# Kernel optimization log

Measured on AMD Instinct MI355X. Metric: run time of the kernel, lower is better.

The kernel has to match this reference:

```python
import jax, jax.numpy as jnp
import numpy as np

B, H, N, D = 4, 16, 2048, 64

def setup_inputs() -> dict:
    key = jax.random.key(0)
    kq, kk, kv = jax.random.split(key, 3)
    q = jax.random.normal(kq, (B, H, N, D), dtype=jnp.float32)
    k = jax.random.normal(kk, (B, H, N, D), dtype=jnp.float32)
    v = jax.random.normal(kv, (B, H, N, D), dtype=jnp.float32)
    return {"q": q, "k": k, "v": v}

def reference(q, k, v):
    scale = q.shape[-1] ** -0.5
    # sim: [b, h, i, j]
    sim = jnp.einsum('bhid,bhjd->bhij', q, k) * scale
    attn = jax.nn.softmax(sim, axis=-1)  # dropout p=0.0 -> identity
    out = jnp.einsum('bhij,bhjd->bhid', attn, v)
    return out
```

## Files before the change

kernel.cpp:

```cpp
#include <hip/hip_runtime.h>
#include <stdint.h>


#define NSEQ 2048
#define DH   64
#define BHN  64
#define NIT  32

typedef short bf16x8 __attribute__((ext_vector_type(8)));
typedef float f32x4  __attribute__((ext_vector_type(4)));
typedef float f32x16 __attribute__((ext_vector_type(16)));

__device__ __forceinline__ uint16_t f2bf(float x) {
    uint32_t u = __builtin_bit_cast(uint32_t, x);
    return (uint16_t)((u + 0x7fffu + ((u >> 16) & 1u)) >> 16);
}
__device__ __forceinline__ uint32_t pk2(float a, float b) {
    return (uint32_t)f2bf(a) | ((uint32_t)f2bf(b) << 16);
}

__global__ __launch_bounds__(256) void prepass(const float* __restrict__ K,
                                               const float* __restrict__ V,
                                               uint16_t* __restrict__ F) {
    __shared__ float T1[64 * 68];
    const int b = blockIdx.x, bh = b >> 5, kt = b & 31, t = threadIdx.x;
    const size_t gbase = ((size_t)bh * NSEQ + (size_t)kt * 64) * DH;
    const int n = t >> 2, d0 = (t & 3) * 16;
    #pragma unroll
    for (int i = 0; i < 4; ++i)
        *(float4*)&T1[n * 68 + d0 + i * 4] = *(const float4*)(V + gbase + n * 64 + d0 + i * 4);
    __syncthreads();
    uint16_t* out = F + (size_t)(bh * 32 + kt) * 8192;
    #pragma unroll
    for (int p = 0; p < 4; ++p) {
        const int e = p * 256 + t, c = e >> 6, l = e & 63;
        const int ll = l & 31, hh = l >> 5;
        float f[8];
        if (c < 8) {
            const int row = (c >> 2) * 32 + ll;
            const int col = hh * 8 + (c & 3) * 16;
            const float* kp = K + gbase + (size_t)row * 64 + col;
            float4 a = *(const float4*)(kp);
            float4 g = *(const float4*)(kp + 4);
            f[0] = a.x; f[1] = a.y; f[2] = a.z; f[3] = a.w;
            f[4] = g.x; f[5] = g.y; f[6] = g.z; f[7] = g.w;
        } else {
            const int cc = c - 8, ktg = cc >> 1;
            const int d = (cc & 1) * 32 + ll;
            #pragma unroll
            for (int j = 0; j < 8; ++j) {
                const int i = hh * 8 + j;
                const int s = (i & 3) + 8 * ((i >> 2) & 1) + 4 * ((i >> 3) & 1);
                f[j] = T1[(ktg * 16 + s) * 68 + d];
            }
        }
        uint4 o = make_uint4(pk2(f[0], f[1]), pk2(f[2], f[3]),
                             pk2(f[4], f[5]), pk2(f[6], f[7]));
        *(uint4*)(out + (size_t)c * 512 + l * 8) = o;
    }
}

__device__ __forceinline__ void load_q(const float* qp, float qscale, bf16x8 (&dst)[4]) {
    #pragma unroll
    for (int k2 = 0; k2 < 4; ++k2) {
        float4 a = *(const float4*)(qp + k2 * 16);
        float4 c = *(const float4*)(qp + k2 * 16 + 4);
        union { uint32_t u[4]; bf16x8 v; } pk;
        pk.u[0] = pk2(a.x * qscale, a.y * qscale);
        pk.u[1] = pk2(a.z * qscale, a.w * qscale);
        pk.u[2] = pk2(c.x * qscale, c.y * qscale);
        pk.u[3] = pk2(c.z * qscale, c.w * qscale);
        dst[k2] = pk.v;
    }
}

__device__ __forceinline__ void tile_mtj(const uint4 (&kc)[4], const uint4 (&vc)[4],
                                         const bf16x8 (&qfn)[4],
                                         f32x16& o0, f32x16& o1, float& lsn) {
    f32x16 s = {};
    #pragma unroll
    for (int k2 = 0; k2 < 4; ++k2)
        s = __builtin_amdgcn_mfma_f32_32x32x16_bf16(
            __builtin_bit_cast(bf16x8, kc[k2]), qfn[k2], s, 0, 0, 0);
    bf16x8 pf0, pf1;
    float g0, g1;
    {
        union { uint32_t u[4]; bf16x8 v; } pp;
        float e[8];
        #pragma unroll
        for (int t2 = 0; t2 < 4; ++t2) {
            e[2 * t2]     = __builtin_amdgcn_exp2f(s[2 * t2]);
            e[2 * t2 + 1] = __builtin_amdgcn_exp2f(s[2 * t2 + 1]);
            pp.u[t2] = __builtin_amdgcn_perm(
                __builtin_bit_cast(uint32_t, e[2 * t2 + 1]),
                __builtin_bit_cast(uint32_t, e[2 * t2]), 0x07060302u);
        }
        g0 = ((e[0] + e[1]) + (e[2] + e[3])) + ((e[4] + e[5]) + (e[6] + e[7]));
        pf0 = pp.v;
    }
    {
        union { uint32_t u[4]; bf16x8 v; } pp;
        float e[8];
        #pragma unroll
        for (int t2 = 0; t2 < 4; ++t2) {
            e[2 * t2]     = __builtin_amdgcn_exp2f(s[8 + 2 * t2]);
            e[2 * t2 + 1] = __builtin_amdgcn_exp2f(s[8 + 2 * t2 + 1]);
            pp.u[t2] = __builtin_amdgcn_perm(
                __builtin_bit_cast(uint32_t, e[2 * t2 + 1]),
                __builtin_bit_cast(uint32_t, e[2 * t2]), 0x07060302u);
        }
        g1 = ((e[0] + e[1]) + (e[2] + e[3])) + ((e[4] + e[5]) + (e[6] + e[7]));
        pf1 = pp.v;
    }
    lsn += g0 + g1;
    o0 = __builtin_amdgcn_mfma_f32_32x32x16_bf16(
        pf0, __builtin_bit_cast(bf16x8, vc[0]), o0, 0, 0, 0);
    o0 = __builtin_amdgcn_mfma_f32_32x32x16_bf16(
        pf1, __builtin_bit_cast(bf16x8, vc[2]), o0, 0, 0, 0);
    o1 = __builtin_amdgcn_mfma_f32_32x32x16_bf16(
        pf0, __builtin_bit_cast(bf16x8, vc[1]), o1, 0, 0, 0);
    o1 = __builtin_amdgcn_mfma_f32_32x32x16_bf16(
        pf1, __builtin_bit_cast(bf16x8, vc[3]), o1, 0, 0, 0);
}

__device__ __forceinline__ void ep_write(float* Ob, int row0,
                                         const f32x16& a0, const f32x16& a1,
                                         float lt, int l31, int h) {
    const float rinv = 1.0f / lt;
    const int rib = __builtin_bit_cast(int, rinv);
    #pragma unroll
    for (int rg = 0; rg < 16; ++rg) {
        const int il = (rg & 3) + 8 * (rg >> 2) + 4 * h;
        const float inv = __builtin_bit_cast(float,
            __builtin_amdgcn_ds_bpermute(il * 4, rib));
        const int row = row0 + il;
        Ob[(size_t)row * DH + l31]      = a0[rg] * inv;
        Ob[(size_t)row * DH + 32 + l31] = a1[rg] * inv;
    }
}

__global__ __launch_bounds__(128, 3) void attn_main(const float* __restrict__ Qg,
                                                    const uint16_t* __restrict__ F,
                                                    float* __restrict__ Og) {
    const int tid = threadIdx.x;
    const int w = tid >> 6, lane = tid & 63;
    const int l31 = lane & 31, h = lane >> 5;
    const int idx = blockIdx.x;
    const int bh = (idx & 7) * 8 + ((idx >> 3) & 7);
    const int qt = idx >> 6;

    const float qscale = 0.125f * 1.44269504f;
    bf16x8 qf[4];
    load_q(Qg + ((size_t)bh * NSEQ + (size_t)(qt * 64 + w * 32 + l31)) * DH + h * 8,
           qscale, qf);

    f32x16 oa0 = {}, oa1 = {};
    float ls = 0.0f;

    const uint16_t* fb = F + (size_t)bh * 32 * 8192 + (size_t)lane * 8;

    #pragma unroll 1
    for (int kt = 0; kt < NIT; ++kt) {
        uint4 kcl[4], kch[4], vcl[4], vch[4];
        #pragma unroll
        for (int c = 0; c < 4; ++c) kcl[c] = *(const uint4*)(fb + (size_t)c * 512);
        #pragma unroll
        for (int c = 0; c < 4; ++c) kch[c] = *(const uint4*)(fb + (size_t)(4 + c) * 512);
        #pragma unroll
        for (int c = 0; c < 4; ++c) vcl[c] = *(const uint4*)(fb + (size_t)(8 + c) * 512);
        #pragma unroll
        for (int c = 0; c < 4; ++c) vch[c] = *(const uint4*)(fb + (size_t)(12 + c) * 512);
        fb += 8192;
        tile_mtj(kcl, vcl, qf, oa0, oa1, ls);
        tile_mtj(kch, vch, qf, oa0, oa1, ls);
    }

    float lt = ls + __shfl_xor(ls, 32);
    float* Ob = Og + (size_t)bh * NSEQ * DH;
    ep_write(Ob, qt * 64 + w * 32, oa0, oa1, lt, l31, h);
}

#define LDS_S 72
#define NWAVE 4
#define BN    64
__global__ __launch_bounds__(256) void attn_fwd_fb(const float* __restrict__ Qg,
                                                   const float* __restrict__ Kg,
                                                   const float* __restrict__ Vg,
                                                   float* __restrict__ Og) {
    __shared__ short KsF[BN * LDS_S];
    __shared__ short VtsF[DH * LDS_S];
    __shared__ short PsF[NWAVE * 16 * LDS_S];
    const int tid = threadIdx.x;
    const int wave = tid >> 6, lane = tid & 63, quad = lane >> 4, l16 = lane & 15;
    const int bh = blockIdx.x >> 5, qtf = blockIdx.x & 31;
    const size_t base = (size_t)bh * NSEQ * DH;
    const float* Qb = Qg + base; const float* Kbf = Kg + base;
    const float* Vb = Vg + base; float* Ob = Og + base;
    const float qscale = 0.125f * 1.44269504f;
    bf16x8 qfrag[2];
    {
        const int qrow = qtf * 64 + wave * 16 + l16;
        const float* qp = Qb + (size_t)qrow * DH + quad * 8;
        #pragma unroll
        for (int c = 0; c < 2; ++c) {
            float4 x = *(const float4*)(qp + 32 * c);
            float4 y = *(const float4*)(qp + 32 * c + 4);
            union { uint16_t u[8]; bf16x8 v; } pk;
            pk.u[0]=f2bf(x.x*qscale); pk.u[1]=f2bf(x.y*qscale);
            pk.u[2]=f2bf(x.z*qscale); pk.u[3]=f2bf(x.w*qscale);
            pk.u[4]=f2bf(y.x*qscale); pk.u[5]=f2bf(y.y*qscale);
            pk.u[6]=f2bf(y.z*qscale); pk.u[7]=f2bf(y.w*qscale);
            qfrag[c] = pk.v;
        }
    }
    f32x4 o[4] = {};
    float m_i[4], l_i[4];
    #pragma unroll
    for (int r = 0; r < 4; ++r) { m_i[r] = -1e30f; l_i[r] = 0.0f; }
    const int kr0 = tid >> 4, kd0 = (tid & 15) * 4;
    const int vp = (tid & 31) * 2, vd0 = (tid >> 5) * 8;
    #pragma unroll 1
    for (int kt = 0; kt < NSEQ / BN; ++kt) {
        __syncthreads();
        {
            const float* kbase = Kbf + (size_t)kt * BN * DH;
            #pragma unroll
            for (int jj = 0; jj < 4; ++jj) {
                const int row = kr0 + jj * 16;
                float4 x = *(const float4*)(kbase + (size_t)row * DH + kd0);
                union { uint16_t u[4]; uint64_t ll; } pk;
                pk.u[0]=f2bf(x.x); pk.u[1]=f2bf(x.y); pk.u[2]=f2bf(x.z); pk.u[3]=f2bf(x.w);
                *(uint64_t*)&KsF[row * LDS_S + kd0] = pk.ll;
            }
        }
        {
            const float* v0 = Vb + (size_t)(kt * BN + vp) * DH + vd0;
            const float* v1 = v0 + DH;
            float4 a0 = *(const float4*)(v0); float4 a1 = *(const float4*)(v0 + 4);
            float4 b0 = *(const float4*)(v1); float4 b1 = *(const float4*)(v1 + 4);
            float av[8] = {a0.x,a0.y,a0.z,a0.w,a1.x,a1.y,a1.z,a1.w};
            float bv[8] = {b0.x,b0.y,b0.z,b0.w,b1.x,b1.y,b1.z,b1.w};
            #pragma unroll
            for (int i = 0; i < 8; ++i)
                *(uint32_t*)&VtsF[(vd0 + i) * LDS_S + vp] = pk2(av[i], bv[i]);
        }
        __syncthreads();
        f32x4 s[4] = {};
        #pragma unroll
        for (int c = 0; c < 2; ++c)
            #pragma unroll
            for (int n = 0; n < 4; ++n) {
                bf16x8 kfr = *(const bf16x8*)&KsF[(n * 16 + l16) * LDS_S + quad * 8 + 32 * c];
                s[n] = __builtin_amdgcn_mfma_f32_16x16x32_bf16(qfrag[c], kfr, s[n], 0, 0, 0);
            }
        float rmax[4];
        #pragma unroll
        for (int r = 0; r < 4; ++r)
            rmax[r] = fmaxf(fmaxf(s[0][r], s[1][r]), fmaxf(s[2][r], s[3][r]));
        #pragma unroll
        for (int off = 1; off < 16; off <<= 1)
            #pragma unroll
            for (int r = 0; r < 4; ++r)
                rmax[r] = fmaxf(rmax[r], __shfl_xor(rmax[r], off, 64));
        float alpha[4], rsum[4];
        #pragma unroll
        for (int r = 0; r < 4; ++r) {
            float mn = fmaxf(m_i[r], rmax[r]);
            alpha[r] = __builtin_amdgcn_exp2f(m_i[r] - mn);
            m_i[r] = mn; rsum[r] = 0.0f;
        }
        #pragma unroll
        for (int n = 0; n < 4; ++n)
            #pragma unroll
            for (int r = 0; r < 4; ++r) {
                float p = __builtin_amdgcn_exp2f(s[n][r] - m_i[r]);
                rsum[r] += p;
                PsF[(wave * 16 + quad * 4 + r) * LDS_S + n * 16 + l16] = (short)f2bf(p);
            }
        #pragma unroll
        for (int off = 1; off < 16; off <<= 1)
            #pragma unroll
            for (int r = 0; r < 4; ++r)
                rsum[r] += __shfl_xor(rsum[r], off, 64);
        #pragma unroll
        for (int r = 0; r < 4; ++r) l_i[r] = l_i[r] * alpha[r] + rsum[r];
        #pragma unroll
        for (int n = 0; n < 4; ++n)
            #pragma unroll
            for (int r = 0; r < 4; ++r) o[n][r] *= alpha[r];
        #pragma unroll
        for (int c = 0; c < 2; ++c) {
            bf16x8 pfr = *(const bf16x8*)&PsF[(wave * 16 + l16) * LDS_S + quad * 8 + 32 * c];
            #pragma unroll
            for (int n = 0; n < 4; ++n) {
                bf16x8 vfr = *(const bf16x8*)&VtsF[(n * 16 + l16) * LDS_S + quad * 8 + 32 * c];
                o[n] = __builtin_amdgcn_mfma_f32_16x16x32_bf16(pfr, vfr, o[n], 0, 0, 0);
            }
        }
    }
    float inv[4];
    #pragma unroll
    for (int r = 0; r < 4; ++r) inv[r] = 1.0f / l_i[r];
    const int orow0 = qtf * 64 + wave * 16 + quad * 4;
    #pragma unroll
    for (int n = 0; n < 4; ++n)
        #pragma unroll
        for (int r = 0; r < 4; ++r)
            Ob[(size_t)(orow0 + r) * DH + n * 16 + l16] = o[n][r] * inv[r];
}

extern "C" void kernel_launch(void* const* d_in, const int* in_sizes, int n_in,
                              void* d_out, int out_size, void* d_ws, size_t ws_size,
                              hipStream_t stream) {
    (void)in_sizes; (void)n_in; (void)out_size;
    const float* q = (const float*)d_in[0];
    const float* k = (const float*)d_in[1];
    const float* v = (const float*)d_in[2];
    float* out = (float*)d_out;
    const size_t need = (size_t)BHN * 32 * 16384;
    if (ws_size >= need) {
        uint16_t* fbuf = (uint16_t*)d_ws;
        prepass<<<dim3(BHN * 32), dim3(256), 0, stream>>>(k, v, fbuf);
        attn_main<<<dim3(2048), dim3(128), 0, stream>>>(q, fbuf, out);
    } else {
        attn_fwd_fb<<<dim3(BHN * 32), dim3(256), 0, stream>>>(q, k, v, out);
    }
}
```

Measured before the change: 208.3 us.

## Share K/V tiles across four waves via double-buffered LDS async loads

The main attention kernel now uses 256-thread blocks covering 128 query rows. Previously each wave read the packed K/V tiles straight from global memory into registers. Now the four waves cooperatively stage each tile into LDS with global_load_lds, double-buffered so the next tile's load overlaps compute on the current one. This cuts redundant global/L2 traffic by sharing each tile across four waves, at the cost of two barriers per iteration, 32KB of LDS per block, and half as many blocks.

```diff
diff --git a/kernel.cpp b/kernel.cpp
--- a/kernel.cpp
+++ b/kernel.cpp
@@ -139,45 +139,69 @@
     }
 }
 
-__global__ __launch_bounds__(128, 3) void attn_main(const float* __restrict__ Qg,
+__device__ __forceinline__ void stage_tile(uint16_t* sb, const uint16_t* ft,
+                                           int w, int lane) {
+    #pragma unroll
+    for (int j = 0; j < 4; ++j) {
+        const int c = w * 4 + j;
+        __builtin_amdgcn_global_load_lds(
+            (const __attribute__((address_space(1))) void*)(ft + (size_t)c * 512 + (size_t)lane * 8),
+            (__attribute__((address_space(3))) void*)(sb + c * 512),
+            16, 0, 0);
+    }
+}
+
+__global__ __launch_bounds__(256, 4) void attn_main(const float* __restrict__ Qg,
                                                     const uint16_t* __restrict__ F,
                                                     float* __restrict__ Og) {
+    __shared__ __align__(16) uint16_t SB[2][8192];
     const int tid = threadIdx.x;
     const int w = tid >> 6, lane = tid & 63;
     const int l31 = lane & 31, h = lane >> 5;
     const int idx = blockIdx.x;
     const int bh = (idx & 7) * 8 + ((idx >> 3) & 7);
-    const int qt = idx >> 6;
+    const int qt2 = idx >> 6;
 
     const float qscale = 0.125f * 1.44269504f;
     bf16x8 qf[4];
-    load_q(Qg + ((size_t)bh * NSEQ + (size_t)(qt * 64 + w * 32 + l31)) * DH + h * 8,
+    load_q(Qg + ((size_t)bh * NSEQ + (size_t)(qt2 * 128 + w * 32 + l31)) * DH + h * 8,
            qscale, qf);
 
     f32x16 oa0 = {}, oa1 = {};
     float ls = 0.0f;
 
-    const uint16_t* fb = F + (size_t)bh * 32 * 8192 + (size_t)lane * 8;
-
+    const uint16_t* fbase = F + (size_t)bh * 32 * 8192;
+
+    stage_tile(&SB[0][0], fbase, w, lane);
     #pragma unroll 1
     for (int kt = 0; kt < NIT; ++kt) {
+        if (kt + 1 < NIT) {
+            stage_tile(&SB[(kt + 1) & 1][0], fbase + (size_t)(kt + 1) * 8192, w, lane);
+            asm volatile("s_waitcnt vmcnt(4)" ::: "memory");
+        } else {
+            asm volatile("s_waitcnt vmcnt(0)" ::: "memory");
+        }
+        __builtin_amdgcn_s_barrier();
+        __builtin_amdgcn_sched_barrier(0);
+        const uint16_t* sb = &SB[kt & 1][0];
         uint4 kcl[4], kch[4], vcl[4], vch[4];
         #pragma unroll
-        for (int c = 0; c < 4; ++c) kcl[c] = *(const uint4*)(fb + (size_t)c * 512);
-        #pragma unroll
-        for (int c = 0; c < 4; ++c) kch[c] = *(const uint4*)(fb + (size_t)(4 + c) * 512);
-        #pragma unroll
-        for (int c = 0; c < 4; ++c) vcl[c] = *(const uint4*)(fb + (size_t)(8 + c) * 512);
-        #pragma unroll
-        for (int c = 0; c < 4; ++c) vch[c] = *(const uint4*)(fb + (size_t)(12 + c) * 512);
-        fb += 8192;
+        for (int c = 0; c < 4; ++c) kcl[c] = *(const uint4*)(sb + (c) * 512 + lane * 8);
+        #pragma unroll
+        for (int c = 0; c < 4; ++c) kch[c] = *(const uint4*)(sb + (4 + c) * 512 + lane * 8);
+        #pragma unroll
+        for (int c = 0; c < 4; ++c) vcl[c] = *(const uint4*)(sb + (8 + c) * 512 + lane * 8);
+        #pragma unroll
+        for (int c = 0; c < 4; ++c) vch[c] = *(const uint4*)(sb + (12 + c) * 512 + lane * 8);
         tile_mtj(kcl, vcl, qf, oa0, oa1, ls);
         tile_mtj(kch, vch, qf, oa0, oa1, ls);
+        __builtin_amdgcn_sched_barrier(0);
+        __builtin_amdgcn_s_barrier();
     }
 
     float lt = ls + __shfl_xor(ls, 32);
     float* Ob = Og + (size_t)bh * NSEQ * DH;
-    ep_write(Ob, qt * 64 + w * 32, oa0, oa1, lt, l31, h);
+    ep_write(Ob, qt2 * 128 + w * 32, oa0, oa1, lt, l31, h);
 }
 
 #define LDS_S 72
@@ -321,7 +345,7 @@
     if (ws_size >= need) {
         uint16_t* fbuf = (uint16_t*)d_ws;
         prepass<<<dim3(BHN * 32), dim3(256), 0, stream>>>(k, v, fbuf);
-        attn_main<<<dim3(2048), dim3(128), 0, stream>>>(q, fbuf, out);
+        attn_main<<<dim3(1024), dim3(256), 0, stream>>>(q, fbuf, out);
     } else {
         attn_fwd_fb<<<dim3(BHN * 32), dim3(256), 0, stream>>>(q, k, v, out);
     }
```

Measured after the change: 199.3 us. 1.05x faster.
